# Kernel tuning notes

Hardware: AMD Instinct MI355X
Metric: run time of the kernel (lower is better)

The kernel has to match this reference:

```python
import jax, jax.numpy as jnp
import numpy as np

N_NODES = 100000
DROP_P = 0.2


def _degree_norm(idx, n):
    deg = jax.ops.segment_sum(jnp.ones_like(idx, dtype=jnp.float32), idx, num_segments=n)
    return jnp.maximum(deg, 1.0) ** -0.5


def gcn_layer(x, src, dst, W, b, n):
    # DGL GraphConv, norm='both', in_feats > out_feats so weight is applied first.
    norm_src = _degree_norm(src, n)  # out-degree^{-1/2}
    norm_dst = _degree_norm(dst, n)  # in-degree^{-1/2}
    h = (x * norm_src[:, None]) @ W            # [N, d_out]
    agg = jax.ops.segment_sum(h[src], dst, num_segments=n)  # gather-scatter over edges
    return agg * norm_dst[:, None] + b


def setup_inputs() -> dict:
    key = jax.random.key(0)
    k = jax.random.split(key, 5)
    x = jax.random.normal(k[0], (N_NODES, 256), dtype=jnp.float32)
    edge_index = jax.random.randint(k[1], (2, 1600000), 0, N_NODES, dtype=jnp.int64)
    W1 = jax.random.normal(k[2], (256, 128), dtype=jnp.float32) * (1.0 / np.sqrt(256))
    b1 = jnp.zeros((128,), dtype=jnp.float32)
    W2 = jax.random.normal(k[3], (128, 47), dtype=jnp.float32) * (1.0 / np.sqrt(128))
    b2 = jnp.zeros((47,), dtype=jnp.float32)
    return {"x": x, "edge_index": edge_index, "W1": W1, "b1": b1, "W2": W2, "b2": b2}


def reference(x, edge_index, W1, b1, W2, b2):
    src, dst = edge_index[0], edge_index[1]
    n = x.shape[0]
    # CRD: GraphConv -> relu -> dropout (F.dropout default training=True; fixed mask)
    h = gcn_layer(x, src, dst, W1, b1, n)
    h = jax.nn.relu(h)
    keep = jax.random.bernoulli(jax.random.key(42), 1.0 - DROP_P, h.shape)
    h = jnp.where(keep, h / (1.0 - DROP_P), 0.0)
    # CLS: GraphConv -> log_softmax over class dim
    out = gcn_layer(h, src, dst, W2, b2, n)
    return jax.nn.log_softmax(out, axis=-1)
```

## Files before the change

### kernel.cpp

```cpp
#include <hip/hip_runtime.h>
#include <math.h>


#define NF0 256
#define NF1 128
#define NC  47
#define CB  1024

typedef __attribute__((ext_vector_type(8))) short bfrag;
typedef __attribute__((ext_vector_type(4))) float f32x4;

__device__ __forceinline__ unsigned short f2bf(float f) {
  unsigned u = __float_as_uint(f);
  return (unsigned short)((u + 0x7fffu + ((u >> 16) & 1u)) >> 16);
}
__device__ __forceinline__ unsigned pack2bf(float a, float b) {
  return (unsigned)f2bf(a) | ((unsigned)f2bf(b) << 16);
}
__device__ __forceinline__ float bflo(unsigned v) { return __uint_as_float(v << 16); }
__device__ __forceinline__ float bfhi(unsigned v) { return __uint_as_float(v & 0xffff0000u); }
__device__ __forceinline__ float bf2f(unsigned short b) {
  return __uint_as_float((unsigned)b << 16);
}

__device__ __forceinline__ unsigned rotl_(unsigned x, int n) {
  return (x << n) | (x >> (32 - n));
}
__device__ __forceinline__ void threefry2x32_(unsigned x0, unsigned x1,
                                              unsigned& o0, unsigned& o1) {
  const unsigned k0 = 0u, k1 = 42u;
  const unsigned k2 = k0 ^ k1 ^ 0x1BD11BDAu;
  x0 += k0; x1 += k1;
  x0+=x1; x1=rotl_(x1,13); x1^=x0;
  x0+=x1; x1=rotl_(x1,15); x1^=x0;
  x0+=x1; x1=rotl_(x1,26); x1^=x0;
  x0+=x1; x1=rotl_(x1, 6); x1^=x0;
  x0+=k1; x1+=k2+1u;
  x0+=x1; x1=rotl_(x1,17); x1^=x0;
  x0+=x1; x1=rotl_(x1,29); x1^=x0;
  x0+=x1; x1=rotl_(x1,16); x1^=x0;
  x0+=x1; x1=rotl_(x1,24); x1^=x0;
  x0+=k2; x1+=k0+2u;
  x0+=x1; x1=rotl_(x1,13); x1^=x0;
  x0+=x1; x1=rotl_(x1,15); x1^=x0;
  x0+=x1; x1=rotl_(x1,26); x1^=x0;
  x0+=x1; x1=rotl_(x1, 6); x1^=x0;
  x0+=k0; x1+=k1+3u;
  x0+=x1; x1=rotl_(x1,17); x1^=x0;
  x0+=x1; x1=rotl_(x1,29); x1^=x0;
  x0+=x1; x1=rotl_(x1,16); x1^=x0;
  x0+=x1; x1=rotl_(x1,24); x1^=x0;
  x0+=k1; x1+=k2+4u;
  x0+=x1; x1=rotl_(x1,13); x1^=x0;
  x0+=x1; x1=rotl_(x1,15); x1^=x0;
  x0+=x1; x1=rotl_(x1,26); x1^=x0;
  x0+=x1; x1=rotl_(x1, 6); x1^=x0;
  x0+=k2; x1+=k0+5u;
  o0 = x0; o1 = x1;
}
__device__ __forceinline__ unsigned dropout_bit(unsigned j) {
  unsigned o0, o1;
  threefry2x32_(0u, j, o0, o1);
  unsigned bits = o0 ^ o1;
  float u = __uint_as_float((bits >> 9) | 0x3f800000u) - 1.0f;
  return (u < 0.8f) ? 1u : 0u;
}


__global__ __launch_bounds__(256) void k_chist(const int* __restrict__ ei, int E,
                                               int nbk, int N, int wblk,
                                               unsigned* __restrict__ bCntD,
                                               unsigned* __restrict__ bCntS,
                                               const float* __restrict__ W1,
                                               const float* __restrict__ W2,
                                               unsigned* __restrict__ W1t32,
                                               unsigned* __restrict__ W2t32,
                                               unsigned* __restrict__ bmask) {
  if ((int)blockIdx.x >= 256 + wblk) {
    int i = (blockIdx.x - 256 - wblk) * 256 + threadIdx.x;
    if (i < 4 * N) {
      unsigned w = 0;
      #pragma unroll 4
      for (int tbit = 0; tbit < 32; tbit++)
        w |= dropout_bit(32u * (unsigned)i + (unsigned)tbit) << tbit;
      bmask[i] = w;
    }
    return;
  }
  if (blockIdx.x >= 256) {
    int i = (blockIdx.x - 256) * 256 + threadIdx.x;
    if (i < 128 * 128) {
      int n = i >> 7, k = (i & 127) << 1;
      W1t32[i] = pack2bf(W1[(size_t)k * NF1 + n], W1[(size_t)(k + 1) * NF1 + n]);
    } else if (i < 128 * 128 + 48 * 64) {
      int j = i - 128 * 128;
      int f = j >> 6, k = (j & 63) << 1;
      float a = (f < NC) ? W2[(size_t)k * NC + f] : 0.f;
      float c = (f < NC) ? W2[(size_t)(k + 1) * NC + f] : 0.f;
      W2t32[j] = pack2bf(a, c);
    }
    return;
  }
  __shared__ unsigned hd[128], hs[128];
  for (int i = threadIdx.x; i < 128; i += 256) { hd[i] = 0; hs[i] = 0; }
  __syncthreads();
  for (int e = blockIdx.x * 256 + threadIdx.x; e < E; e += 256 * 256) {
    int s = ei[e], d = ei[E + e];
    atomicAdd(&hs[s >> 10], 1u);
    atomicAdd(&hd[d >> 10], 1u);
  }
  __syncthreads();
  for (int i = threadIdx.x; i < nbk; i += 256) {
    if (hd[i]) atomicAdd(&bCntD[i], hd[i]);
    if (hs[i]) atomicAdd(&bCntS[i], hs[i]);
  }
}

__global__ __launch_bounds__(256) void k_cscatter(const int* __restrict__ ei, int E,
                                                  const unsigned* __restrict__ bCntD,
                                                  const unsigned* __restrict__ bCntS,
                                                  unsigned* __restrict__ curD,
                                                  unsigned* __restrict__ curS,
                                                  unsigned* __restrict__ pd,
                                                  unsigned short* __restrict__ ps,
                                                  int nbk) {
  __shared__ unsigned hd[128], hs[128];
  __shared__ unsigned baseD[128], baseS[128];
  __shared__ unsigned sc[256];
  const int t = threadIdx.x;
  int per = (E + gridDim.x - 1) / gridDim.x;
  int e0 = blockIdx.x * per;
  int e1 = min(e0 + per, E);
  unsigned orig = (t < 128) ? ((t < nbk) ? bCntD[t] : 0u)
                            : (((t - 128) < nbk) ? bCntS[t - 128] : 0u);
  sc[t] = orig;
  if (t < 128) { hd[t] = 0; hs[t] = 0; }
  __syncthreads();
  for (int e = e0 + t; e < e1; e += 256) {
    int s = ei[e], d = ei[E + e];
    atomicAdd(&hs[s >> 10], 1u);
    atomicAdd(&hd[d >> 10], 1u);
  }
  __syncthreads();
  #pragma unroll
  for (int o = 1; o < 128; o <<= 1) {
    unsigned u = ((t & 127) >= o) ? sc[t - o] : 0u;
    __syncthreads();
    sc[t] += u;
    __syncthreads();
  }
  if (t < 128) {
    unsigned excl = sc[t] - orig;
    unsigned h = hd[t];
    baseD[t] = excl + (h ? atomicAdd(&curD[t], h) : 0u);
    hd[t] = 0;
  } else {
    int i = t - 128;
    unsigned excl = sc[t] - orig;
    unsigned h = hs[i];
    baseS[i] = excl + (h ? atomicAdd(&curS[i], h) : 0u);
    hs[i] = 0;
  }
  __syncthreads();
  for (int e = e0 + t; e < e1; e += 256) {
    int s = ei[e], d = ei[E + e];
    int bd = d >> 10, bs = s >> 10;
    unsigned pD = baseD[bd] + atomicAdd(&hd[bd], 1u);
    unsigned pS = baseS[bs] + atomicAdd(&hs[bs], 1u);
    pd[pD] = ((unsigned)(d & (CB - 1)) << 17) | (unsigned)s;
    ps[pS] = (unsigned short)(s & (CB - 1));
  }
}

__global__ __launch_bounds__(256) void k_fine(const unsigned* __restrict__ bCntD,
                                              const unsigned* __restrict__ bCntS,
                                              const unsigned* __restrict__ pd,
                                              const unsigned short* __restrict__ ps,
                                              unsigned* __restrict__ off,
                                              float* __restrict__ norm_dst,
                                              float* __restrict__ norm_src,
                                              int* __restrict__ csr,
                                              int N, int E, int nbk) {
  __shared__ unsigned cnt[CB];
  __shared__ unsigned part[256];
  __shared__ unsigned sc[256];
  const int t = threadIdx.x;
  const bool isD = (int)blockIdx.x < nbk;
  const int b = isD ? (int)blockIdx.x : ((int)blockIdx.x - nbk);
  unsigned orig = (t < 128) ? ((t < nbk) ? bCntD[t] : 0u)
                            : (((t - 128) < nbk) ? bCntS[t - 128] : 0u);
  sc[t] = orig;
  __syncthreads();
  #pragma unroll
  for (int o = 1; o < 128; o <<= 1) {
    unsigned u = ((t & 127) >= o) ? sc[t - o] : 0u;
    __syncthreads();
    sc[t] += u;
    __syncthreads();
  }
  const int idx = isD ? b : (128 + b);
  const unsigned hi = sc[idx];
  const unsigned lo = hi - (isD ? bCntD[b] : bCntS[b]);
  const int base = b << 10;
  for (int i = t; i < CB; i += 256) cnt[i] = 0;
  __syncthreads();
  if (isD) {
    for (unsigned j = lo + t; j < hi; j += 256) atomicAdd(&cnt[pd[j] >> 17], 1u);
    __syncthreads();
    unsigned c0 = cnt[4*t], c1 = cnt[4*t+1], c2 = cnt[4*t+2], c3 = cnt[4*t+3];
    unsigned tsum = c0 + c1 + c2 + c3;
    part[t] = tsum;
    __syncthreads();
    #pragma unroll
    for (int o = 1; o < 256; o <<= 1) {
      unsigned u = (t >= o) ? part[t - o] : 0u;
      __syncthreads();
      part[t] += u;
      __syncthreads();
    }
    unsigned e0 = part[t] - tsum;
    unsigned p0 = e0, p1 = e0 + c0, p2 = p1 + c1, p3 = p2 + c2;
    int n0 = base + 4 * t;
    if (n0 + 0 < N) { off[n0+0] = lo + p0; norm_dst[n0+0] = 1.0f / sqrtf((float)(c0 < 1u ? 1u : c0)); }
    if (n0 + 1 < N) { off[n0+1] = lo + p1; norm_dst[n0+1] = 1.0f / sqrtf((float)(c1 < 1u ? 1u : c1)); }
    if (n0 + 2 < N) { off[n0+2] = lo + p2; norm_dst[n0+2] = 1.0f / sqrtf((float)(c2 < 1u ? 1u : c2)); }
    if (n0 + 3 < N) { off[n0+3] = lo + p3; norm_dst[n0+3] = 1.0f / sqrtf((float)(c3 < 1u ? 1u : c3)); }
    if (b == nbk - 1 && t == 0) off[N] = (unsigned)E;
    __syncthreads();
    cnt[4*t] = p0; cnt[4*t+1] = p1; cnt[4*t+2] = p2; cnt[4*t+3] = p3;
    __syncthreads();
    for (unsigned j = lo + t; j < hi; j += 256) {
      unsigned v = pd[j];
      unsigned pos = atomicAdd(&cnt[v >> 17], 1u);
      csr[lo + pos] = (int)(v & 0x1FFFFu);
    }
  } else {
    for (unsigned j = lo + t; j < hi; j += 256) atomicAdd(&cnt[ps[j]], 1u);
    __syncthreads();
    for (int i = t; i < CB; i += 256) {
      int n = base + i;
      if (n < N) {
        unsigned c = cnt[i];
        norm_src[n] = 1.0f / sqrtf((float)(c < 1u ? 1u : c));
      }
    }
  }
}

__global__ __launch_bounds__(256) void k_gemm1(const float* __restrict__ x,
                                               const unsigned* __restrict__ W1t32,
                                               const float* __restrict__ norm_src,
                                               unsigned short* __restrict__ h1, int N) {
  __shared__ unsigned As[128][20];
  __shared__ unsigned Bs[128][20];
  const int m0 = blockIdx.x * 128;
  const int t = threadIdx.x;
  const int lane = t & 63, wid = t >> 6;
  const int fr = lane & 15, ko = (lane >> 4) * 8;

  f32x4 acc[2][8];
  #pragma unroll
  for (int r = 0; r < 2; r++)
    #pragma unroll
    for (int c = 0; c < 8; c++) acc[r][c] = (f32x4){0.f, 0.f, 0.f, 0.f};

  const int sr = t >> 1;
  const int shw = (t & 1) * 8;

  for (int k0 = 0; k0 < NF0; k0 += 32) {
    {
      unsigned w[8];
      int gm = m0 + sr;
      if (gm < N) {
        const float* p = x + (size_t)gm * NF0 + k0 + shw * 2;
        #pragma unroll
        for (int q = 0; q < 4; q++) {
          float4 v = *(const float4*)(p + q * 4);
          w[2*q]   = pack2bf(v.x, v.y);
          w[2*q+1] = pack2bf(v.z, v.w);
        }
      } else {
        #pragma unroll
        for (int q = 0; q < 8; q++) w[q] = 0u;
      }
      *(uint4*)&As[sr][shw]     = make_uint4(w[0], w[1], w[2], w[3]);
      *(uint4*)&As[sr][shw + 4] = make_uint4(w[4], w[5], w[6], w[7]);
    }
    {
      const unsigned* pb = W1t32 + (size_t)sr * (NF0 / 2) + (k0 >> 1) + shw;
      *(uint4*)&Bs[sr][shw]     = *(const uint4*)pb;
      *(uint4*)&Bs[sr][shw + 4] = *(const uint4*)(pb + 4);
    }
    __syncthreads();
    const unsigned short* As16 = (const unsigned short*)&As[0][0];
    const unsigned short* Bs16 = (const unsigned short*)&Bs[0][0];
    #pragma unroll
    for (int r = 0; r < 2; r++) {
      bfrag a = *(const bfrag*)(As16 + (size_t)(wid * 32 + r * 16 + fr) * 40 + ko);
      #pragma unroll
      for (int c = 0; c < 8; c++) {
        bfrag b = *(const bfrag*)(Bs16 + (size_t)(c * 16 + fr) * 40 + ko);
        acc[r][c] = __builtin_amdgcn_mfma_f32_16x16x32_bf16(a, b, acc[r][c], 0, 0, 0);
      }
    }
    __syncthreads();
  }

  #pragma unroll
  for (int r = 0; r < 2; r++) {
    int rbase = m0 + wid * 32 + r * 16 + (lane >> 4) * 4;
    float ns[4];
    #pragma unroll
    for (int g = 0; g < 4; g++) ns[g] = (rbase + g < N) ? norm_src[rbase + g] : 0.f;
    #pragma unroll
    for (int c = 0; c < 8; c++) {
      int col = c * 16 + fr;
      #pragma unroll
      for (int g = 0; g < 4; g++) {
        int row = rbase + g;
        if (row < N) h1[(size_t)row * NF1 + col] = f2bf(acc[r][c][g] * ns[g]);
      }
    }
  }
}

__global__ __launch_bounds__(256) void k_gather1(const unsigned* __restrict__ off,
                                                 const int* __restrict__ csr,
                                                 const unsigned short* __restrict__ h1,
                                                 const float* __restrict__ norm_dst,
                                                 const float* __restrict__ norm_src,
                                                 const float* __restrict__ b1,
                                                 const unsigned* __restrict__ bmask,
                                                 unsigned* __restrict__ h2, int N) {
  const int t = threadIdx.x;
  const int lane = t & 63, wid = t >> 6;
  const int eg = lane >> 4;
  const int q  = lane & 15;
  const int ngroups = (N + 3) >> 2;
  const float4 bA = *(const float4*)(b1 + q * 8);
  const float4 bB = *(const float4*)(b1 + q * 8 + 4);

  for (int grp = blockIdx.x; grp < ngroups; grp += gridDim.x) {
    int node = grp * 4 + wid;
    if (node >= N) continue;
    unsigned j = off[node], e1 = off[node + 1];
    float ax0=0.f, ax1=0.f, ax2=0.f, ax3=0.f;
    float ay0=0.f, ay1=0.f, ay2=0.f, ay3=0.f;
    for (; j + 4 <= e1; j += 4) {
      int s = csr[j + eg];
      uint4 v = *(const uint4*)(h1 + (size_t)s * NF1 + q * 8);
      ax0 += bflo(v.x); ay0 += bfhi(v.x);
      ax1 += bflo(v.y); ay1 += bfhi(v.y);
      ax2 += bflo(v.z); ay2 += bfhi(v.z);
      ax3 += bflo(v.w); ay3 += bfhi(v.w);
    }
    if (j < e1) {
      unsigned rem = e1 - j;
      if ((unsigned)eg < rem) {
        int s = csr[j + eg];
        uint4 v = *(const uint4*)(h1 + (size_t)s * NF1 + q * 8);
        ax0 += bflo(v.x); ay0 += bfhi(v.x);
        ax1 += bflo(v.y); ay1 += bfhi(v.y);
        ax2 += bflo(v.z); ay2 += bfhi(v.z);
        ax3 += bflo(v.w); ay3 += bfhi(v.w);
      }
    }
    ax0 += __shfl_xor(ax0, 16); ax0 += __shfl_xor(ax0, 32);
    ay0 += __shfl_xor(ay0, 16); ay0 += __shfl_xor(ay0, 32);
    ax1 += __shfl_xor(ax1, 16); ax1 += __shfl_xor(ax1, 32);
    ay1 += __shfl_xor(ay1, 16); ay1 += __shfl_xor(ay1, 32);
    ax2 += __shfl_xor(ax2, 16); ax2 += __shfl_xor(ax2, 32);
    ay2 += __shfl_xor(ay2, 16); ay2 += __shfl_xor(ay2, 32);
    ax3 += __shfl_xor(ax3, 16); ax3 += __shfl_xor(ax3, 32);
    ay3 += __shfl_xor(ay3, 16); ay3 += __shfl_xor(ay3, 32);
    if (eg == 0) {
      float nd = norm_dst[node], ns = norm_src[node];
      unsigned mw = bmask[node * 4 + (q >> 2)];
      unsigned mb = (mw >> ((q & 3) * 8)) & 0xffu;
      float v0 = fmaxf(ax0 * nd + bA.x, 0.f);
      float v1 = fmaxf(ay0 * nd + bA.y, 0.f);
      float v2 = fmaxf(ax1 * nd + bA.z, 0.f);
      float v3 = fmaxf(ay1 * nd + bA.w, 0.f);
      float v4 = fmaxf(ax2 * nd + bB.x, 0.f);
      float v5 = fmaxf(ay2 * nd + bB.y, 0.f);
      float v6 = fmaxf(ax3 * nd + bB.z, 0.f);
      float v7 = fmaxf(ay3 * nd + bB.w, 0.f);
      v0 *= ((mb >> 0) & 1 ? 1.25f : 0.f) * ns;
      v1 *= ((mb >> 1) & 1 ? 1.25f : 0.f) * ns;
      v2 *= ((mb >> 2) & 1 ? 1.25f : 0.f) * ns;
      v3 *= ((mb >> 3) & 1 ? 1.25f : 0.f) * ns;
      v4 *= ((mb >> 4) & 1 ? 1.25f : 0.f) * ns;
      v5 *= ((mb >> 5) & 1 ? 1.25f : 0.f) * ns;
      v6 *= ((mb >> 6) & 1 ? 1.25f : 0.f) * ns;
      v7 *= ((mb >> 7) & 1 ? 1.25f : 0.f) * ns;
      uint4 o;
      o.x = pack2bf(v0, v1);
      o.y = pack2bf(v2, v3);
      o.z = pack2bf(v4, v5);
      o.w = pack2bf(v6, v7);
      *(uint4*)(h2 + (size_t)node * 64 + q * 4) = o;
    }
  }
}

__global__ __launch_bounds__(256) void k_gemm2(const unsigned* __restrict__ h2,
                                               const unsigned* __restrict__ W2t32,
                                               unsigned short* __restrict__ g, int N) {
  const int t = threadIdx.x;
  const int lane = t & 63, wid = t >> 6;
  const int fr = lane & 15, hi4 = lane >> 4;
  const int row = blockIdx.x * 64 + wid * 16 + fr;

  bfrag a[4];
  const unsigned* ap = h2 + (size_t)row * 64 + hi4 * 4;
  #pragma unroll
  for (int kk = 0; kk < 4; kk++) {
    uint4 v = *(const uint4*)(ap + kk * 16);
    a[kk] = *(bfrag*)&v;
  }

  const int rbase = blockIdx.x * 64 + wid * 16 + hi4 * 4;
  #pragma unroll
  for (int c = 0; c < 3; c++) {
    f32x4 acc = (f32x4){0.f, 0.f, 0.f, 0.f};
    const unsigned* bp = W2t32 + (size_t)(c * 16 + fr) * 64 + hi4 * 4;
    #pragma unroll
    for (int kk = 0; kk < 4; kk++) {
      uint4 w = *(const uint4*)(bp + kk * 16);
      bfrag b = *(bfrag*)&w;
      acc = __builtin_amdgcn_mfma_f32_16x16x32_bf16(a[kk], b, acc, 0, 0, 0);
    }
    int col = c * 16 + fr;
    #pragma unroll
    for (int r = 0; r < 4; r++) {
      int nr = rbase + r;
      if (nr < N) g[(size_t)nr * 48 + col] = f2bf(acc[r]);
    }
  }
}

__global__ __launch_bounds__(256) void k_gather2(const unsigned* __restrict__ off,
                                                 const int* __restrict__ csr,
                                                 const unsigned short* __restrict__ g,
                                                 const float* __restrict__ norm_dst,
                                                 const float* __restrict__ b2,
                                                 float* __restrict__ out, int N) {
  int node = (blockIdx.x * 256 + threadIdx.x) >> 6;
  int lane = threadIdx.x & 63;
  if (node >= N) return;
  unsigned j = off[node], e1 = off[node + 1];
  float acc = 0.f;
  for (; j + 4 <= e1; j += 4) {
    int s0 = csr[j], s1 = csr[j+1], s2 = csr[j+2], s3 = csr[j+3];
    if (lane < 48) {
      float a0 = bf2f(g[(size_t)s0 * 48 + lane]);
      float a1 = bf2f(g[(size_t)s1 * 48 + lane]);
      float a2 = bf2f(g[(size_t)s2 * 48 + lane]);
      float a3 = bf2f(g[(size_t)s3 * 48 + lane]);
      acc += (a0 + a1) + (a2 + a3);
    }
  }
  for (; j < e1; j++) {
    if (lane < 48) acc += bf2f(g[(size_t)csr[j] * 48 + lane]);
  }
  float nd = norm_dst[node];
  float vr = 0.f, m = -INFINITY;
  if (lane < NC) {
    vr = acc * nd + b2[lane];
    m = vr;
  }
  #pragma unroll
  for (int o = 32; o; o >>= 1) m = fmaxf(m, __shfl_xor(m, o));
  float ex = (lane < NC) ? expf(vr - m) : 0.f;
  #pragma unroll
  for (int o = 32; o; o >>= 1) ex += __shfl_xor(ex, o);
  float ls = logf(ex);
  if (lane < NC) out[(size_t)node * NC + lane] = vr - m - ls;
}

extern "C" void kernel_launch(void* const* d_in, const int* in_sizes, int n_in,
                              void* d_out, int out_size, void* d_ws, size_t ws_size,
                              hipStream_t stream) {
  const float* x  = (const float*)d_in[0];
  const int*   ei = (const int*)d_in[1];
  const float* W1 = (const float*)d_in[2];
  const float* b1 = (const float*)d_in[3];
  const float* W2 = (const float*)d_in[4];
  const float* b2 = (const float*)d_in[5];
  float* out = (float*)d_out;

  const int N = in_sizes[0] / NF0;
  const int E = in_sizes[1] / 2;
  const int nbk = (N + CB - 1) / CB;
  const int Npad = (N + 63) & ~63;

  unsigned* ws = (unsigned*)d_ws;
  size_t o = 0;
  auto alloc = [&](size_t elems) { size_t p = o; o += (elems + 3) & ~(size_t)3; return p; };
  float*    norm_src = (float*)(ws + alloc(N));
  float*    norm_dst = (float*)(ws + alloc(N));
  unsigned* off      = ws + alloc(N + 1);
  unsigned* bCntD    = ws + alloc(128);
  unsigned* bCntS    = ws + alloc(128);
  unsigned* curD     = ws + alloc(128);
  unsigned* curS     = ws + alloc(128);
  unsigned* bmask    = ws + alloc((size_t)4 * N);
  unsigned* pd       = ws + alloc(E);
  unsigned short* ps = (unsigned short*)(ws + alloc(E / 2));
  int*      csr      = (int*)(ws + alloc(E));
  unsigned* W1t32    = ws + alloc(128 * 128);
  unsigned* W2t32    = ws + alloc(48 * 64);
  unsigned short* h1 = (unsigned short*)(ws + alloc((size_t)N * NF1 / 2));
  unsigned* h2       = ws + alloc((size_t)Npad * 64);
  unsigned short* gbuf;
  if ((size_t)E * 3 >= (size_t)N * 48) {
    gbuf = (unsigned short*)pd;
  } else {
    gbuf = (unsigned short*)(ws + alloc(((size_t)N * 48 + 1) / 2));
  }

  hipMemsetAsync(bCntD, 0, 512 * sizeof(unsigned), stream);

  int wblk = (128 * 128 + 48 * 64 + 255) / 256;
  int mblk = (4 * N + 255) / 256;
  k_chist<<<256 + wblk + mblk, 256, 0, stream>>>(ei, E, nbk, N, wblk, bCntD, bCntS,
                                                 W1, W2, W1t32, W2t32, bmask);
  k_cscatter<<<256, 256, 0, stream>>>(ei, E, bCntD, bCntS, curD, curS, pd, ps, nbk);
  k_fine<<<2 * nbk, 256, 0, stream>>>(bCntD, bCntS, pd, ps, off, norm_dst, norm_src,
                                      csr, N, E, nbk);
  k_gemm1<<<(N + 127) / 128, 256, 0, stream>>>(x, W1t32, norm_src, h1, N);
  k_gather1<<<2048, 256, 0, stream>>>(off, csr, h1, norm_dst, norm_src, b1, bmask,
                                      h2, N);
  k_gemm2<<<Npad / 64, 256, 0, stream>>>(h2, W2t32, gbuf, N);
  k_gather2<<<((size_t)N * 64 + 255) / 256, 256, 0, stream>>>(
      off, csr, gbuf, norm_dst, b2, out, N);
}
```

Baseline: 471.7 us.

## Move dropout mask to k_fine, unroll gather1 by 8, vectorize gather2 with padded rows

Dropout mask generation moves from the histogram kernel into the fine-sort kernel's extra blocks, so the expensive threefry work runs alongside the fine sort rather than the histogram. The first gather unrolls to two independent row loads per iteration, giving more memory-level parallelism. The layer-2 projection is now stored as 64-wide padded bf16 rows reusing the h1 buffer. The second gather reads packed bf16 pairs so each wavefront handles two edges per load, and the log-softmax reductions shrink to 32 lanes.

```diff
diff --git a/kernel.cpp b/kernel.cpp
--- a/kernel.cpp
+++ b/kernel.cpp
@@ -68,25 +68,13 @@
 
 
 __global__ __launch_bounds__(256) void k_chist(const int* __restrict__ ei, int E,
-                                               int nbk, int N, int wblk,
+                                               int nbk,
                                                unsigned* __restrict__ bCntD,
                                                unsigned* __restrict__ bCntS,
                                                const float* __restrict__ W1,
                                                const float* __restrict__ W2,
                                                unsigned* __restrict__ W1t32,
-                                               unsigned* __restrict__ W2t32,
-                                               unsigned* __restrict__ bmask) {
-  if ((int)blockIdx.x >= 256 + wblk) {
-    int i = (blockIdx.x - 256 - wblk) * 256 + threadIdx.x;
-    if (i < 4 * N) {
-      unsigned w = 0;
-      #pragma unroll 4
-      for (int tbit = 0; tbit < 32; tbit++)
-        w |= dropout_bit(32u * (unsigned)i + (unsigned)tbit) << tbit;
-      bmask[i] = w;
-    }
-    return;
-  }
+                                               unsigned* __restrict__ W2t32) {
   if (blockIdx.x >= 256) {
     int i = (blockIdx.x - 256) * 256 + threadIdx.x;
     if (i < 128 * 128) {
@@ -180,11 +168,23 @@
                                               float* __restrict__ norm_dst,
                                               float* __restrict__ norm_src,
                                               int* __restrict__ csr,
-                                              int N, int E, int nbk) {
+                                              int N, int E, int nbk,
+                                              unsigned* __restrict__ bmask) {
+  const int t = threadIdx.x;
+  if ((int)blockIdx.x >= 2 * nbk) {
+    int i = ((int)blockIdx.x - 2 * nbk) * 256 + t;
+    if (i < 4 * N) {
+      unsigned w = 0;
+      #pragma unroll 4
+      for (int tbit = 0; tbit < 32; tbit++)
+        w |= dropout_bit(32u * (unsigned)i + (unsigned)tbit) << tbit;
+      bmask[i] = w;
+    }
+    return;
+  }
   __shared__ unsigned cnt[CB];
   __shared__ unsigned part[256];
   __shared__ unsigned sc[256];
-  const int t = threadIdx.x;
   const bool isD = (int)blockIdx.x < nbk;
   const int b = isD ? (int)blockIdx.x : ((int)blockIdx.x - nbk);
   unsigned orig = (t < 128) ? ((t < nbk) ? bCntD[t] : 0u)
@@ -346,13 +346,24 @@
     unsigned j = off[node], e1 = off[node + 1];
     float ax0=0.f, ax1=0.f, ax2=0.f, ax3=0.f;
     float ay0=0.f, ay1=0.f, ay2=0.f, ay3=0.f;
-    for (; j + 4 <= e1; j += 4) {
+    for (; j + 8 <= e1; j += 8) {
+      int sA = csr[j + eg];
+      int sB = csr[j + 4 + eg];
+      uint4 vA = *(const uint4*)(h1 + (size_t)sA * NF1 + q * 8);
+      uint4 vB = *(const uint4*)(h1 + (size_t)sB * NF1 + q * 8);
+      ax0 += bflo(vA.x) + bflo(vB.x); ay0 += bfhi(vA.x) + bfhi(vB.x);
+      ax1 += bflo(vA.y) + bflo(vB.y); ay1 += bfhi(vA.y) + bfhi(vB.y);
+      ax2 += bflo(vA.z) + bflo(vB.z); ay2 += bfhi(vA.z) + bfhi(vB.z);
+      ax3 += bflo(vA.w) + bflo(vB.w); ay3 += bfhi(vA.w) + bfhi(vB.w);
+    }
+    if (j + 4 <= e1) {
       int s = csr[j + eg];
       uint4 v = *(const uint4*)(h1 + (size_t)s * NF1 + q * 8);
       ax0 += bflo(v.x); ay0 += bfhi(v.x);
       ax1 += bflo(v.y); ay1 += bfhi(v.y);
       ax2 += bflo(v.z); ay2 += bfhi(v.z);
       ax3 += bflo(v.w); ay3 += bfhi(v.w);
+      j += 4;
     }
     if (j < e1) {
       unsigned rem = e1 - j;
@@ -434,48 +445,63 @@
     #pragma unroll
     for (int r = 0; r < 4; r++) {
       int nr = rbase + r;
-      if (nr < N) g[(size_t)nr * 48 + col] = f2bf(acc[r]);
-    }
+      if (nr < N) g[(size_t)nr * 64 + col] = f2bf(acc[r]);
+    }
+  }
+  #pragma unroll
+  for (int r = 0; r < 4; r++) {
+    int nr = rbase + r;
+    if (nr < N) g[(size_t)nr * 64 + 48 + fr] = 0;
   }
 }
 
 __global__ __launch_bounds__(256) void k_gather2(const unsigned* __restrict__ off,
                                                  const int* __restrict__ csr,
-                                                 const unsigned short* __restrict__ g,
+                                                 const unsigned* __restrict__ g64,
                                                  const float* __restrict__ norm_dst,
                                                  const float* __restrict__ b2,
                                                  float* __restrict__ out, int N) {
   int node = (blockIdx.x * 256 + threadIdx.x) >> 6;
   int lane = threadIdx.x & 63;
   if (node >= N) return;
+  const int h = lane >> 5, q = lane & 31;
   unsigned j = off[node], e1 = off[node + 1];
-  float acc = 0.f;
+  float a0 = 0.f, a1 = 0.f;
   for (; j + 4 <= e1; j += 4) {
-    int s0 = csr[j], s1 = csr[j+1], s2 = csr[j+2], s3 = csr[j+3];
-    if (lane < 48) {
-      float a0 = bf2f(g[(size_t)s0 * 48 + lane]);
-      float a1 = bf2f(g[(size_t)s1 * 48 + lane]);
-      float a2 = bf2f(g[(size_t)s2 * 48 + lane]);
-      float a3 = bf2f(g[(size_t)s3 * 48 + lane]);
-      acc += (a0 + a1) + (a2 + a3);
-    }
-  }
-  for (; j < e1; j++) {
-    if (lane < 48) acc += bf2f(g[(size_t)csr[j] * 48 + lane]);
-  }
+    int sA = csr[j + h], sB = csr[j + 2 + h];
+    unsigned vA = g64[(size_t)sA * 32 + q];
+    unsigned vB = g64[(size_t)sB * 32 + q];
+    a0 += bflo(vA) + bflo(vB);
+    a1 += bfhi(vA) + bfhi(vB);
+  }
+  if (j + 2 <= e1) {
+    int s = csr[j + h];
+    unsigned v = g64[(size_t)s * 32 + q];
+    a0 += bflo(v); a1 += bfhi(v);
+    j += 2;
+  }
+  if (j < e1 && h == 0) {
+    int s = csr[j];
+    unsigned v = g64[(size_t)s * 32 + q];
+    a0 += bflo(v); a1 += bfhi(v);
+  }
+  a0 += __shfl_xor(a0, 32);
+  a1 += __shfl_xor(a1, 32);
   float nd = norm_dst[node];
-  float vr = 0.f, m = -INFINITY;
-  if (lane < NC) {
-    vr = acc * nd + b2[lane];
-    m = vr;
-  }
-  #pragma unroll
-  for (int o = 32; o; o >>= 1) m = fmaxf(m, __shfl_xor(m, o));
-  float ex = (lane < NC) ? expf(vr - m) : 0.f;
-  #pragma unroll
-  for (int o = 32; o; o >>= 1) ex += __shfl_xor(ex, o);
+  int f0 = 2 * q, f1 = 2 * q + 1;
+  float v0 = (f0 < NC) ? a0 * nd + b2[f0] : -INFINITY;
+  float v1 = (f1 < NC) ? a1 * nd + b2[f1] : -INFINITY;
+  float m = fmaxf(v0, v1);
+  #pragma unroll
+  for (int o = 16; o; o >>= 1) m = fmaxf(m, __shfl_xor(m, o));
+  float ex = ((f0 < NC) ? expf(v0 - m) : 0.f) + ((f1 < NC) ? expf(v1 - m) : 0.f);
+  #pragma unroll
+  for (int o = 16; o; o >>= 1) ex += __shfl_xor(ex, o);
   float ls = logf(ex);
-  if (lane < NC) out[(size_t)node * NC + lane] = vr - m - ls;
+  if (h == 0) {
+    if (f0 < NC) out[(size_t)node * NC + f0] = v0 - m - ls;
+    if (f1 < NC) out[(size_t)node * NC + f1] = v1 - m - ls;
+  }
 }
 
 extern "C" void kernel_launch(void* const* d_in, const int* in_sizes, int n_in,
@@ -512,26 +538,21 @@
   unsigned* W2t32    = ws + alloc(48 * 64);
   unsigned short* h1 = (unsigned short*)(ws + alloc((size_t)N * NF1 / 2));
   unsigned* h2       = ws + alloc((size_t)Npad * 64);
-  unsigned short* gbuf;
-  if ((size_t)E * 3 >= (size_t)N * 48) {
-    gbuf = (unsigned short*)pd;
-  } else {
-    gbuf = (unsigned short*)(ws + alloc(((size_t)N * 48 + 1) / 2));
-  }
+  unsigned short* g64 = h1;
 
   hipMemsetAsync(bCntD, 0, 512 * sizeof(unsigned), stream);
 
   int wblk = (128 * 128 + 48 * 64 + 255) / 256;
   int mblk = (4 * N + 255) / 256;
-  k_chist<<<256 + wblk + mblk, 256, 0, stream>>>(ei, E, nbk, N, wblk, bCntD, bCntS,
-                                                 W1, W2, W1t32, W2t32, bmask);
+  k_chist<<<256 + wblk, 256, 0, stream>>>(ei, E, nbk, bCntD, bCntS, W1, W2,
+                                          W1t32, W2t32);
   k_cscatter<<<256, 256, 0, stream>>>(ei, E, bCntD, bCntS, curD, curS, pd, ps, nbk);
-  k_fine<<<2 * nbk, 256, 0, stream>>>(bCntD, bCntS, pd, ps, off, norm_dst, norm_src,
-                                      csr, N, E, nbk);
+  k_fine<<<2 * nbk + mblk, 256, 0, stream>>>(bCntD, bCntS, pd, ps, off, norm_dst,
+                                             norm_src, csr, N, E, nbk, bmask);
   k_gemm1<<<(N + 127) / 128, 256, 0, stream>>>(x, W1t32, norm_src, h1, N);
   k_gather1<<<2048, 256, 0, stream>>>(off, csr, h1, norm_dst, norm_src, b1, bmask,
                                       h2, N);
-  k_gemm2<<<Npad / 64, 256, 0, stream>>>(h2, W2t32, gbuf, N);
+  k_gemm2<<<Npad / 64, 256, 0, stream>>>(h2, W2t32, g64, N);
   k_gather2<<<((size_t)N * 64 + 255) / 256, 256, 0, stream>>>(
-      off, csr, gbuf, norm_dst, b2, out, N);
-}
+      off, csr, (const unsigned*)g64, norm_dst, b2, out, N);
+}
```

Result: faster. 457.6 us (-3.0%).
